# Performance work log

Hardware: AMD Instinct MI355X
Metric: run time of the kernel (lower is better)

The kernel has to match this reference:

```python
import jax, jax.numpy as jnp
import numpy as np

N_NODES = 50000
N_EDGES = 600000
VOCAB = 50000
D_IN = 256   # embed.output_size
D = 128      # size


def gcn_conv(x, w, b, src, dst, num_nodes):
    # PyG GCNConv: x' = D^{-1/2} (A + I) D^{-1/2} (x @ W^T) + b
    loop = jnp.arange(num_nodes)
    s = jnp.concatenate([src, loop])
    d = jnp.concatenate([dst, loop])
    x = x @ w.T                                           # [N, D]
    deg = jax.ops.segment_sum(jnp.ones_like(s, x.dtype), d, num_segments=num_nodes)
    dinv = jnp.where(deg > 0, jax.lax.rsqrt(deg), 0.0)
    norm = dinv[s] * dinv[d]                              # [E+N]
    msgs = x[s] * norm[:, None]                           # gather + scale
    out = jax.ops.segment_sum(msgs, d, num_segments=num_nodes)  # scatter-add
    return out + b


def setup_inputs() -> dict:
    key = jax.random.key(0)
    ks = jax.random.split(key, 7)
    node_tokens = jax.random.randint(ks[0], (N_NODES,), 0, VOCAB)
    edge_index = jax.random.randint(ks[1], (2, N_EDGES), 0, N_NODES)
    embed_table = jax.random.normal(ks[2], (VOCAB, D_IN), dtype=jnp.float32) * 0.02
    W_node_w = jax.random.normal(ks[3], (D, D_IN), dtype=jnp.float32) * 0.02
    W_node_b = jnp.zeros((D,), dtype=jnp.float32)
    w1 = jax.random.normal(ks[4], (D, D), dtype=jnp.float32) * 0.02
    b1 = jnp.zeros((D,), dtype=jnp.float32)
    w2 = jax.random.normal(ks[5], (D, D), dtype=jnp.float32) * 0.02
    b2 = jnp.zeros((D,), dtype=jnp.float32)
    return {"node_tokens": node_tokens, "edge_index": edge_index,
            "embed_table": embed_table, "W_node_w": W_node_w, "W_node_b": W_node_b,
            "w1": w1, "b1": b1, "w2": w2, "b2": b2}


def reference(node_tokens, edge_index, embed_table, W_node_w, W_node_b, w1, b1, w2, b2):
    src, dst = edge_index[0], edge_index[1]
    e = embed_table[node_tokens]                 # [N, D_IN] embedding lookup
    x = e @ W_node_w.T + W_node_b                # [N, D]
    x = gcn_conv(x, w1, b1, src, dst, N_NODES)
    x = jax.nn.relu(x)
    x = gcn_conv(x, w2, b2, src, dst, N_NODES)
    return x
```

## Files before the change

### kernel.cpp

```cpp
#include <hip/hip_runtime.h>
#include <hip/hip_bf16.h>

#define N_NODES 50000
#define N_EDGES 600000
#define D_IN 256
#define D 128

#define GEMM_BLOCKS ((N_NODES + 31) / 32)
#define EDGE_BLOCKS ((N_EDGES + 255) / 256)
#define OUT_CHUNKS (N_NODES / 16)
#define BCAP 32
#define OVF_CAP 2048

typedef unsigned short ushort_t;
typedef __attribute__((ext_vector_type(8))) short bf16x8;
typedef __attribute__((ext_vector_type(16))) float f32x16;

__device__ __forceinline__ float bf2f(ushort_t u) {
  union { unsigned int i; float f; } v;
  v.i = ((unsigned int)u) << 16;
  return v.f;
}
__device__ __forceinline__ ushort_t f2bf(float f) {
  union { float f; unsigned int i; } v;
  v.f = f;
  unsigned int x = v.i;
  unsigned int r = (x + 0x7FFFu + ((x >> 16) & 1u)) >> 16;
  return (ushort_t)r;
}
__device__ __forceinline__ float bflo(unsigned int u) {
  union { unsigned int i; float f; } v;
  v.i = u << 16;
  return v.f;
}
__device__ __forceinline__ float bfhi(unsigned int u) {
  union { unsigned int i; float f; } v;
  v.i = u & 0xFFFF0000u;
  return v.f;
}


__global__ __launch_bounds__(256) void k_prep_fill(
    const float* __restrict__ wn, const float* __restrict__ w1,
    const float* __restrict__ bn, const float* __restrict__ w2,
    const float* __restrict__ b1, const float* __restrict__ b2,
    const int* __restrict__ src, const int* __restrict__ dst,
    ushort_t* __restrict__ WcSw, ushort_t* __restrict__ W2Sw,
    float* __restrict__ bias_ws, int* __restrict__ deg,
    int* __restrict__ bucket, int* __restrict__ ovfc, int* __restrict__ ovf,
    ushort_t* __restrict__ T1z, ushort_t* __restrict__ T2z) {
  int bid = blockIdx.x;
  int tid = threadIdx.x;
  float* bcf = bias_ws;
  float* b1f = bias_ws + 128;
  float* b2f = bias_ws + 256;
  if (bid < 128) {
    int j = bid;
    int k = tid;
    float acc = 0.f;
#pragma unroll 8
    for (int m = 0; m < 128; m++)
      acc += w1[j * 128 + m] * wn[m * 256 + k];
    ushort_t h = f2bf(acc);
    ushort_t l = f2bf(acc - bf2f(h));
    int wv = j >> 5, fm = j & 31;
    int kh = k >> 7, t = (k >> 4) & 7, fq = (k >> 3) & 1, c = k & 7;
    int lane = fq * 32 + fm;
    int base = ((wv * 2 + kh) * 8 + t) * 2 * 512 + lane * 8 + c;
    WcSw[base] = h;
    WcSw[base + 512] = l;
    if (k == 0) {
      float s = 0.f;
      for (int m = 0; m < 128; m++) s += w1[j * 128 + m] * bn[m];
      bcf[j] = s;
    }
  } else if (bid < 193) {
    int i = (bid - 128) * 256 + tid;
    if (i < 16384) {
      float v = w2[i];
      ushort_t h = f2bf(v);
      ushort_t l = f2bf(v - bf2f(h));
      int j = i >> 7, k = i & 127;
      int wv = j >> 5, fm = j & 31;
      int t = (k >> 4) & 7, fq = (k >> 3) & 1, c = k & 7;
      int lane = fq * 32 + fm;
      int base = (wv * 8 + t) * 2 * 512 + lane * 8 + c;
      W2Sw[base] = h;
      W2Sw[base + 512] = l;
    } else if (i < 16512) {
      b1f[i - 16384] = b1[i - 16384];
    } else if (i < 16640) {
      b2f[i - 16512] = b2[i - 16512];
    }
  } else if (bid == 193) {
    unsigned int* z1 = (unsigned int*)&T1z[(size_t)N_NODES * D];
    unsigned int* z2 = (unsigned int*)&T2z[(size_t)N_NODES * D];
    if (tid < 64) z1[tid] = 0u;
    else if (tid < 128) z2[tid - 64] = 0u;
  } else {
    int e = (bid - 194) * 256 + tid;
    if (e < N_EDGES) {
      int d = dst[e];
      int s = src[e];
      int pos = atomicAdd(&deg[d], 1);
      if (pos < BCAP) {
        bucket[d * BCAP + pos] = s;
      } else {
        int oi = atomicAdd(ovfc, 1);
        if (oi < OVF_CAP) {
          ovf[2 * oi] = d;
          ovf[2 * oi + 1] = s;
        }
      }
    }
  }
}

__global__ __launch_bounds__(256) void k_gemm(
    const float* __restrict__ Xv, const int* __restrict__ tokens,
    const ushort_t* __restrict__ Wsw, const float* __restrict__ bias,
    const int* __restrict__ deg, ushort_t* __restrict__ OutT) {
  constexpr int XS = 136;
  __shared__ __align__(16) ushort_t xh_lds[32 * XS];
  __shared__ __align__(16) ushort_t xl_lds[32 * XS];

  int tid = threadIdx.x;
  int lane = tid & 63;
  int wv = tid >> 6;
  int node0 = blockIdx.x * 32;
  int fm = lane & 31;
  int fq = lane >> 5;
  int r8 = tid >> 5;
  int c32 = tid & 31;

  const char* xb = (const char*)Xv;
  float4 v0[4], v1[4];
  int rows[4];
#pragma unroll
  for (int i = 0; i < 4; i++) {
    rows[i] = r8 * 4 + i;
    int tk = tokens[min(node0 + rows[i], N_NODES - 1)];
    unsigned off = (unsigned)tk * (D_IN * 4) + (unsigned)c32 * 16;
    v0[i] = *(const float4*)(xb + off);
    v1[i] = *(const float4*)(xb + off + 512);
  }

  f32x16 acc;
#pragma unroll
  for (int r = 0; r < 16; r++) acc[r] = 0.f;

#pragma unroll
  for (int kh = 0; kh < 2; kh++) {
#pragma unroll
    for (int i = 0; i < 4; i++) {
      float4 v = (kh == 0) ? v0[i] : v1[i];
      ushort4 h, l;
      h.x = f2bf(v.x); l.x = f2bf(v.x - bf2f(h.x));
      h.y = f2bf(v.y); l.y = f2bf(v.y - bf2f(h.y));
      h.z = f2bf(v.z); l.z = f2bf(v.z - bf2f(h.z));
      h.w = f2bf(v.w); l.w = f2bf(v.w - bf2f(h.w));
      *(ushort4*)&xh_lds[rows[i] * XS + 4 * c32] = h;
      *(ushort4*)&xl_lds[rows[i] * XS + 4 * c32] = l;
    }
    __syncthreads();

    const ushort_t* wb = Wsw + ((size_t)(wv * 2 + kh) * 8) * 2 * 512 + lane * 8;
#pragma unroll
    for (int tc = 0; tc < 2; tc++) {
      bf16x8 wbh[4], wbl[4];
#pragma unroll
      for (int t4 = 0; t4 < 4; t4++) {
        wbh[t4] = *(const bf16x8*)(wb + (size_t)(tc * 4 + t4) * 1024);
        wbl[t4] = *(const bf16x8*)(wb + (size_t)(tc * 4 + t4) * 1024 + 512);
      }
#pragma unroll
      for (int t4 = 0; t4 < 4; t4++) {
        int ko = (tc * 4 + t4) * 16 + fq * 8;
        bf16x8 ah = *(const bf16x8*)&xh_lds[fm * XS + ko];
        bf16x8 al = *(const bf16x8*)&xl_lds[fm * XS + ko];
        acc = __builtin_amdgcn_mfma_f32_32x32x16_bf16(ah, wbh[t4], acc, 0, 0, 0);
        acc = __builtin_amdgcn_mfma_f32_32x32x16_bf16(ah, wbl[t4], acc, 0, 0, 0);
        acc = __builtin_amdgcn_mfma_f32_32x32x16_bf16(al, wbh[t4], acc, 0, 0, 0);
      }
    }
    if (kh == 0) __syncthreads();
  }

  int j = wv * 32 + fm;
  float bv = bias[j];
#pragma unroll
  for (int r = 0; r < 16; r++) {
    int row = (r & 3) + 8 * (r >> 2) + 4 * fq;
    int node = node0 + row;
    if (node < N_NODES) {
      float di = rsqrtf((float)(deg[node] + 1));
      OutT[(size_t)node * D + j] = f2bf((acc[r] + bv) * di);
    }
  }
}

__device__ __forceinline__ void addu4(float acc[8], uint4 u) {
  acc[0] += bflo(u.x);
  acc[1] += bfhi(u.x);
  acc[2] += bflo(u.y);
  acc[3] += bfhi(u.y);
  acc[4] += bflo(u.z);
  acc[5] += bfhi(u.z);
  acc[6] += bflo(u.w);
  acc[7] += bfhi(u.w);
}

__device__ __forceinline__ uint4 ldrow(const char* tbase, int s, int h) {
  return *(const uint4*)(tbase + (((unsigned)s << 8) + ((unsigned)h << 4)));
}

__device__ __forceinline__ void burst8(const char* tbase, int sidx,
                                       int gbase, int qoff, int h, float acc[8]) {
  uint4 u[8];
#pragma unroll
  for (int q = 0; q < 8; q++) {
    int s = __shfl(sidx, gbase + qoff + q);
    u[q] = ldrow(tbase, s, h);
  }
#pragma unroll
  for (int q = 0; q < 8; q++) addu4(acc, u[q]);
}

__device__ __forceinline__ void gather_node(
    const char* tbase, const int* __restrict__ bucket,
    const int* __restrict__ ovf, int novf,
    int node, int degv, bool valid, int gbase, int h, float acc[8]) {
  int cnt = valid ? min(degv, BCAP) : 0;
  addu4(acc, ldrow(tbase, valid ? node : N_NODES, h));
  int sidx = (h < cnt) ? bucket[node * BCAP + h] : N_NODES;
  burst8(tbase, sidx, gbase, 0, h, acc);
  burst8(tbase, sidx, gbase, 8, h, acc);
  for (int b2 = 16; b2 < cnt; b2 += 16) {
    int sx = (b2 + h < cnt) ? bucket[node * BCAP + b2 + h] : N_NODES;
    burst8(tbase, sx, gbase, 0, h, acc);
    burst8(tbase, sx, gbase, 8, h, acc);
  }
  if (valid && degv > BCAP) {
    for (int i = 0; i < novf; i++) {
      if (ovf[2 * i] == node) addu4(acc, ldrow(tbase, ovf[2 * i + 1], h));
    }
  }
}

__global__ __launch_bounds__(256) void k_agg_gemm(
    const ushort_t* __restrict__ t1, const int* __restrict__ deg,
    const int* __restrict__ bucket, const int* __restrict__ ovfc,
    const int* __restrict__ ovf, const float* __restrict__ b1f,
    const ushort_t* __restrict__ Wsw, ushort_t* __restrict__ OutT2) {
  constexpr int XS = 136;
  __shared__ __align__(16) ushort_t xh_lds[32 * XS];
  __shared__ __align__(16) ushort_t xl_lds[32 * XS];

  int tid = threadIdx.x;
  int lane = tid & 63;
  int wv = tid >> 6;
  int node0 = blockIdx.x * 32;
  int fm = lane & 31;
  int fq = lane >> 5;
  int g = lane >> 4;
  int h = lane & 15;
  int gbase = lane & 48;

  const char* tb = (const char*)t1;
  float4 bA = *(const float4*)&b1f[h * 8];
  float4 bB = *(const float4*)&b1f[h * 8 + 4];
  int novf = *ovfc;

  int node0w = node0 + wv * 8;
  int dgl = deg[min(node0w + min(lane, 7), N_NODES - 1)];

  int nodeA = node0w + g;
  int nodeB = node0w + 4 + g;
  int degA = __shfl(dgl, g);
  int degB = __shfl(dgl, 4 + g);
  bool vA = nodeA < N_NODES, vB = nodeB < N_NODES;
  float diA = rsqrtf((float)(degA + 1));
  float diB = rsqrtf((float)(degB + 1));

  float accA[8];
#pragma unroll
  for (int q = 0; q < 8; q++) accA[q] = 0.f;
  gather_node(tb, bucket, ovf, novf, nodeA, degA, vA, gbase, h, accA);

  float accB[8];
#pragma unroll
  for (int q = 0; q < 8; q++) accB[q] = 0.f;
  gather_node(tb, bucket, ovf, novf, nodeB, degB, vB, gbase, h, accB);

#pragma unroll
  for (int p = 0; p < 2; p++) {
    float* acc = p ? accB : accA;
    bool vv = p ? vB : vA;
    float di = p ? diB : diA;
    int row = wv * 8 + p * 4 + g;
    bf16x8 ph, pl;
    if (vv) {
      float val[8];
      val[0] = fmaxf(di * acc[0] + bA.x, 0.f);
      val[1] = fmaxf(di * acc[1] + bA.y, 0.f);
      val[2] = fmaxf(di * acc[2] + bA.z, 0.f);
      val[3] = fmaxf(di * acc[3] + bA.w, 0.f);
      val[4] = fmaxf(di * acc[4] + bB.x, 0.f);
      val[5] = fmaxf(di * acc[5] + bB.y, 0.f);
      val[6] = fmaxf(di * acc[6] + bB.z, 0.f);
      val[7] = fmaxf(di * acc[7] + bB.w, 0.f);
#pragma unroll
      for (int q = 0; q < 8; q++) {
        ushort_t hq = f2bf(val[q]);
        ph[q] = (short)hq;
        pl[q] = (short)f2bf(val[q] - bf2f(hq));
      }
    } else {
#pragma unroll
      for (int q = 0; q < 8; q++) { ph[q] = 0; pl[q] = 0; }
    }
    *(bf16x8*)&xh_lds[row * XS + h * 8] = ph;
    *(bf16x8*)&xl_lds[row * XS + h * 8] = pl;
  }
  __syncthreads();

  f32x16 acc;
#pragma unroll
  for (int r = 0; r < 16; r++) acc[r] = 0.f;
  {
    const ushort_t* wb = Wsw + ((size_t)wv * 8) * 2 * 512 + lane * 8;
#pragma unroll
    for (int tc = 0; tc < 2; tc++) {
      bf16x8 wbh[4], wbl[4];
#pragma unroll
      for (int t4 = 0; t4 < 4; t4++) {
        wbh[t4] = *(const bf16x8*)(wb + (size_t)(tc * 4 + t4) * 1024);
        wbl[t4] = *(const bf16x8*)(wb + (size_t)(tc * 4 + t4) * 1024 + 512);
      }
#pragma unroll
      for (int t4 = 0; t4 < 4; t4++) {
        int ko = (tc * 4 + t4) * 16 + fq * 8;
        bf16x8 ah = *(const bf16x8*)&xh_lds[fm * XS + ko];
        bf16x8 al = *(const bf16x8*)&xl_lds[fm * XS + ko];
        acc = __builtin_amdgcn_mfma_f32_32x32x16_bf16(ah, wbh[t4], acc, 0, 0, 0);
        acc = __builtin_amdgcn_mfma_f32_32x32x16_bf16(ah, wbl[t4], acc, 0, 0, 0);
        acc = __builtin_amdgcn_mfma_f32_32x32x16_bf16(al, wbh[t4], acc, 0, 0, 0);
      }
    }
  }
  int j = wv * 32 + fm;
#pragma unroll
  for (int r = 0; r < 16; r++) {
    int row = (r & 3) + 8 * (r >> 2) + 4 * fq;
    int node = node0 + row;
    if (node < N_NODES) {
      float di = rsqrtf((float)(deg[node] + 1));
      OutT2[(size_t)node * D + j] = f2bf(acc[r] * di);
    }
  }
}

__global__ __launch_bounds__(256) void k_agg_out(
    const ushort_t* __restrict__ t, const int* __restrict__ deg,
    const int* __restrict__ bucket, const int* __restrict__ ovfc,
    const int* __restrict__ ovf, const float* __restrict__ bias,
    float* __restrict__ out_f) {
  int wv = threadIdx.x >> 6;
  int lane = threadIdx.x & 63;
  int g = lane >> 4;
  int h = lane & 15;
  int gbase = lane & 48;
  int nodew = blockIdx.x * 16 + wv * 4;
  int dgl = deg[min(nodew + min(lane, 3), N_NODES - 1)];
  int node = nodew + g;
  int degn = __shfl(dgl, g);
  bool vn = node < N_NODES;
  float di = rsqrtf((float)(degn + 1));
  int novf = *ovfc;

  const char* tb = (const char*)t;
  float acc[8];
#pragma unroll
  for (int q = 0; q < 8; q++) acc[q] = 0.f;
  gather_node(tb, bucket, ovf, novf, node, degn, vn, gbase, h, acc);

  if (!vn) return;
  float4 bA = *(const float4*)&bias[h * 8];
  float4 bB = *(const float4*)&bias[h * 8 + 4];
  float4 o0, o1;
  o0.x = di * acc[0] + bA.x;
  o0.y = di * acc[1] + bA.y;
  o0.z = di * acc[2] + bA.z;
  o0.w = di * acc[3] + bA.w;
  o1.x = di * acc[4] + bB.x;
  o1.y = di * acc[5] + bB.y;
  o1.z = di * acc[6] + bB.z;
  o1.w = di * acc[7] + bB.w;
  *(float4*)&out_f[(size_t)node * D + h * 8] = o0;
  *(float4*)&out_f[(size_t)node * D + h * 8 + 4] = o1;
}

extern "C" void kernel_launch(void* const* d_in, const int* in_sizes, int n_in,
                              void* d_out, int out_size, void* d_ws, size_t ws_size,
                              hipStream_t stream) {
  const int* tokens = (const int*)d_in[0];
  const int* edge = (const int*)d_in[1];
  const float* embed = (const float*)d_in[2];
  const float* Wn = (const float*)d_in[3];
  const float* bn = (const float*)d_in[4];
  const float* w1 = (const float*)d_in[5];
  const float* b1 = (const float*)d_in[6];
  const float* w2 = (const float*)d_in[7];
  const float* b2 = (const float*)d_in[8];
  float* out = (float*)d_out;

  const int* src = edge;
  const int* dst = edge + N_EDGES;

  char* ws = (char*)d_ws;
  ushort_t* T1 = (ushort_t*)ws;
  ushort_t* T2 = (ushort_t*)(ws + 12800256);
  int* bucket = (int*)(ws + 25600512);
  int* deg = (int*)(ws + 32000512);
  int* ovfc = (int*)(ws + 32200512);
  int* ovf = (int*)(ws + 32200640);
  ushort_t* WcSw = (ushort_t*)(ws + 32217088);
  ushort_t* W2Sw = (ushort_t*)(ws + 32348160);
  float* bias_ws = (float*)(ws + 32413696);
  float* bcf = bias_ws;
  float* b1f = bias_ws + 128;
  float* b2f = bias_ws + 256;

  hipMemsetAsync(deg, 0, 200128, stream);

  k_prep_fill<<<194 + EDGE_BLOCKS, 256, 0, stream>>>(
      Wn, w1, bn, w2, b1, b2, src, dst, WcSw, W2Sw, bias_ws, deg,
      bucket, ovfc, ovf, T1, T2);

  k_gemm<<<GEMM_BLOCKS, 256, 0, stream>>>(
      embed, tokens, WcSw, bcf, deg, T1);

  k_agg_gemm<<<GEMM_BLOCKS, 256, 0, stream>>>(
      T1, deg, bucket, ovfc, ovf, b1f, W2Sw, T2);

  k_agg_out<<<OUT_CHUNKS, 256, 0, stream>>>(
      T2, deg, bucket, ovfc, ovf, b2f, out);
}
```

Baseline: 227.9 us.

## Fuse bucket fill into first GEMM and move degree scaling to gather

The edge-bucketing pass is merged into the embedding GEMM kernel using interleaved block roles, so the atomic scatter runs concurrently with the MFMA work instead of as a separate serial stage. Because the GEMM no longer has degree counts available, the source-side rsqrt(deg) normalization moves into the gather as a per-neighbor FMA scale. Bucket entries are stored as 16-bit indices to halve index traffic. This adds per-edge deg lookups and shuffles in the aggregation, and the 16-bit indices rely on node ids fitting in 16 bits. Since 50000 is below 65536 that holds, though the code does not check it.

```diff
diff --git a/kernel.cpp b/kernel.cpp
--- a/kernel.cpp
+++ b/kernel.cpp
@@ -8,6 +8,7 @@
 
 #define GEMM_BLOCKS ((N_NODES + 31) / 32)
 #define EDGE_BLOCKS ((N_EDGES + 255) / 256)
+#define MIX_BLOCKS 3910
 #define OUT_CHUNKS (N_NODES / 16)
 #define BCAP 32
 #define OVF_CAP 2048
@@ -40,14 +41,12 @@
 }
 
 
-__global__ __launch_bounds__(256) void k_prep_fill(
+__global__ __launch_bounds__(256) void k_wprep(
     const float* __restrict__ wn, const float* __restrict__ w1,
     const float* __restrict__ bn, const float* __restrict__ w2,
     const float* __restrict__ b1, const float* __restrict__ b2,
-    const int* __restrict__ src, const int* __restrict__ dst,
     ushort_t* __restrict__ WcSw, ushort_t* __restrict__ W2Sw,
-    float* __restrict__ bias_ws, int* __restrict__ deg,
-    int* __restrict__ bucket, int* __restrict__ ovfc, int* __restrict__ ovf,
+    float* __restrict__ bias_ws,
     ushort_t* __restrict__ T1z, ushort_t* __restrict__ T2z) {
   int bid = blockIdx.x;
   int tid = threadIdx.x;
@@ -92,19 +91,38 @@
     } else if (i < 16640) {
       b2f[i - 16512] = b2[i - 16512];
     }
-  } else if (bid == 193) {
+  } else {
     unsigned int* z1 = (unsigned int*)&T1z[(size_t)N_NODES * D];
     unsigned int* z2 = (unsigned int*)&T2z[(size_t)N_NODES * D];
     if (tid < 64) z1[tid] = 0u;
     else if (tid < 128) z2[tid - 64] = 0u;
-  } else {
-    int e = (bid - 194) * 256 + tid;
+  }
+}
+
+__global__ __launch_bounds__(256) void k_gemm_fill(
+    const float* __restrict__ Xv, const int* __restrict__ tokens,
+    const ushort_t* __restrict__ Wsw, const float* __restrict__ bias,
+    ushort_t* __restrict__ OutT,
+    const int* __restrict__ src, const int* __restrict__ dst,
+    int* __restrict__ deg, ushort_t* __restrict__ bucket,
+    int* __restrict__ ovfc, int* __restrict__ ovf) {
+  constexpr int XS = 136;
+  __shared__ __align__(16) ushort_t xh_lds[32 * XS];
+  __shared__ __align__(16) ushort_t xl_lds[32 * XS];
+
+  int bid = blockIdx.x;
+  int tid = threadIdx.x;
+  int grp = bid / 5, r = bid % 5;
+  if (r >= 2) {
+    int c = grp * 3 + (r - 2);
+    if (c >= EDGE_BLOCKS) return;
+    int e = c * 256 + tid;
     if (e < N_EDGES) {
       int d = dst[e];
       int s = src[e];
       int pos = atomicAdd(&deg[d], 1);
       if (pos < BCAP) {
-        bucket[d * BCAP + pos] = s;
+        bucket[d * BCAP + pos] = (ushort_t)s;
       } else {
         int oi = atomicAdd(ovfc, 1);
         if (oi < OVF_CAP) {
@@ -113,21 +131,14 @@
         }
       }
     }
-  }
-}
-
-__global__ __launch_bounds__(256) void k_gemm(
-    const float* __restrict__ Xv, const int* __restrict__ tokens,
-    const ushort_t* __restrict__ Wsw, const float* __restrict__ bias,
-    const int* __restrict__ deg, ushort_t* __restrict__ OutT) {
-  constexpr int XS = 136;
-  __shared__ __align__(16) ushort_t xh_lds[32 * XS];
-  __shared__ __align__(16) ushort_t xl_lds[32 * XS];
-
-  int tid = threadIdx.x;
+    return;
+  }
+
+  int t = grp * 2 + r;
+  if (t >= GEMM_BLOCKS) return;
   int lane = tid & 63;
   int wv = tid >> 6;
-  int node0 = blockIdx.x * 32;
+  int node0 = t * 32;
   int fm = lane & 31;
   int fq = lane >> 5;
   int r8 = tid >> 5;
@@ -147,7 +158,7 @@
 
   f32x16 acc;
 #pragma unroll
-  for (int r = 0; r < 16; r++) acc[r] = 0.f;
+  for (int q = 0; q < 16; q++) acc[q] = 0.f;
 
 #pragma unroll
   for (int kh = 0; kh < 2; kh++) {
@@ -189,67 +200,71 @@
   int j = wv * 32 + fm;
   float bv = bias[j];
 #pragma unroll
-  for (int r = 0; r < 16; r++) {
-    int row = (r & 3) + 8 * (r >> 2) + 4 * fq;
+  for (int q = 0; q < 16; q++) {
+    int row = (q & 3) + 8 * (q >> 2) + 4 * fq;
     int node = node0 + row;
-    if (node < N_NODES) {
-      float di = rsqrtf((float)(deg[node] + 1));
-      OutT[(size_t)node * D + j] = f2bf((acc[r] + bv) * di);
-    }
-  }
-}
-
-__device__ __forceinline__ void addu4(float acc[8], uint4 u) {
-  acc[0] += bflo(u.x);
-  acc[1] += bfhi(u.x);
-  acc[2] += bflo(u.y);
-  acc[3] += bfhi(u.y);
-  acc[4] += bflo(u.z);
-  acc[5] += bfhi(u.z);
-  acc[6] += bflo(u.w);
-  acc[7] += bfhi(u.w);
+    if (node < N_NODES)
+      OutT[(size_t)node * D + j] = f2bf(acc[q] + bv);
+  }
+}
+
+__device__ __forceinline__ void fma8(float acc[8], uint4 u, float f) {
+  acc[0] = fmaf(bflo(u.x), f, acc[0]);
+  acc[1] = fmaf(bfhi(u.x), f, acc[1]);
+  acc[2] = fmaf(bflo(u.y), f, acc[2]);
+  acc[3] = fmaf(bfhi(u.y), f, acc[3]);
+  acc[4] = fmaf(bflo(u.z), f, acc[4]);
+  acc[5] = fmaf(bfhi(u.z), f, acc[5]);
+  acc[6] = fmaf(bflo(u.w), f, acc[6]);
+  acc[7] = fmaf(bfhi(u.w), f, acc[7]);
 }
 
 __device__ __forceinline__ uint4 ldrow(const char* tbase, int s, int h) {
   return *(const uint4*)(tbase + (((unsigned)s << 8) + ((unsigned)h << 4)));
 }
 
-__device__ __forceinline__ void burst8(const char* tbase, int sidx,
-                                       int gbase, int qoff, int h, float acc[8]) {
+__device__ __forceinline__ void burst8s(const char* tbase, int sidx, float scl,
+                                        int gbase, int qoff, int h, float acc[8]) {
   uint4 u[8];
+  float f[8];
 #pragma unroll
   for (int q = 0; q < 8; q++) {
     int s = __shfl(sidx, gbase + qoff + q);
+    f[q] = __shfl(scl, gbase + qoff + q);
     u[q] = ldrow(tbase, s, h);
   }
 #pragma unroll
-  for (int q = 0; q < 8; q++) addu4(acc, u[q]);
+  for (int q = 0; q < 8; q++) fma8(acc, u[q], f[q]);
 }
 
 __device__ __forceinline__ void gather_node(
-    const char* tbase, const int* __restrict__ bucket,
-    const int* __restrict__ ovf, int novf,
+    const char* tbase, const ushort_t* __restrict__ bucket,
+    const int* __restrict__ deg, const int* __restrict__ ovf, int novf,
     int node, int degv, bool valid, int gbase, int h, float acc[8]) {
   int cnt = valid ? min(degv, BCAP) : 0;
-  addu4(acc, ldrow(tbase, valid ? node : N_NODES, h));
-  int sidx = (h < cnt) ? bucket[node * BCAP + h] : N_NODES;
-  burst8(tbase, sidx, gbase, 0, h, acc);
-  burst8(tbase, sidx, gbase, 8, h, acc);
+  int sidx = (h < cnt) ? (int)bucket[node * BCAP + h] : N_NODES;
+  float scl = rsqrtf((float)(deg[sidx] + 1));
+  burst8s(tbase, sidx, scl, gbase, 0, h, acc);
+  burst8s(tbase, sidx, scl, gbase, 8, h, acc);
   for (int b2 = 16; b2 < cnt; b2 += 16) {
-    int sx = (b2 + h < cnt) ? bucket[node * BCAP + b2 + h] : N_NODES;
-    burst8(tbase, sx, gbase, 0, h, acc);
-    burst8(tbase, sx, gbase, 8, h, acc);
+    int sx = (b2 + h < cnt) ? (int)bucket[node * BCAP + b2 + h] : N_NODES;
+    float sc = rsqrtf((float)(deg[sx] + 1));
+    burst8s(tbase, sx, sc, gbase, 0, h, acc);
+    burst8s(tbase, sx, sc, gbase, 8, h, acc);
   }
   if (valid && degv > BCAP) {
     for (int i = 0; i < novf; i++) {
-      if (ovf[2 * i] == node) addu4(acc, ldrow(tbase, ovf[2 * i + 1], h));
+      if (ovf[2 * i] == node) {
+        int s = ovf[2 * i + 1];
+        fma8(acc, ldrow(tbase, s, h), rsqrtf((float)(deg[s] + 1)));
+      }
     }
   }
 }
 
 __global__ __launch_bounds__(256) void k_agg_gemm(
     const ushort_t* __restrict__ t1, const int* __restrict__ deg,
-    const int* __restrict__ bucket, const int* __restrict__ ovfc,
+    const ushort_t* __restrict__ bucket, const int* __restrict__ ovfc,
     const int* __restrict__ ovf, const float* __restrict__ b1f,
     const ushort_t* __restrict__ Wsw, ushort_t* __restrict__ OutT2) {
   constexpr int XS = 136;
@@ -285,12 +300,14 @@
   float accA[8];
 #pragma unroll
   for (int q = 0; q < 8; q++) accA[q] = 0.f;
-  gather_node(tb, bucket, ovf, novf, nodeA, degA, vA, gbase, h, accA);
+  fma8(accA, ldrow(tb, vA ? nodeA : N_NODES, h), diA);
+  gather_node(tb, bucket, deg, ovf, novf, nodeA, degA, vA, gbase, h, accA);
 
   float accB[8];
 #pragma unroll
   for (int q = 0; q < 8; q++) accB[q] = 0.f;
-  gather_node(tb, bucket, ovf, novf, nodeB, degB, vB, gbase, h, accB);
+  fma8(accB, ldrow(tb, vB ? nodeB : N_NODES, h), diB);
+  gather_node(tb, bucket, deg, ovf, novf, nodeB, degB, vB, gbase, h, accB);
 
 #pragma unroll
   for (int p = 0; p < 2; p++) {
@@ -326,7 +343,7 @@
 
   f32x16 acc;
 #pragma unroll
-  for (int r = 0; r < 16; r++) acc[r] = 0.f;
+  for (int q = 0; q < 16; q++) acc[q] = 0.f;
   {
     const ushort_t* wb = Wsw + ((size_t)wv * 8) * 2 * 512 + lane * 8;
 #pragma unroll
@@ -350,19 +367,17 @@
   }
   int j = wv * 32 + fm;
 #pragma unroll
-  for (int r = 0; r < 16; r++) {
-    int row = (r & 3) + 8 * (r >> 2) + 4 * fq;
+  for (int q = 0; q < 16; q++) {
+    int row = (q & 3) + 8 * (q >> 2) + 4 * fq;
     int node = node0 + row;
-    if (node < N_NODES) {
-      float di = rsqrtf((float)(deg[node] + 1));
-      OutT2[(size_t)node * D + j] = f2bf(acc[r] * di);
-    }
+    if (node < N_NODES)
+      OutT2[(size_t)node * D + j] = f2bf(acc[q]);
   }
 }
 
 __global__ __launch_bounds__(256) void k_agg_out(
     const ushort_t* __restrict__ t, const int* __restrict__ deg,
-    const int* __restrict__ bucket, const int* __restrict__ ovfc,
+    const ushort_t* __restrict__ bucket, const int* __restrict__ ovfc,
     const int* __restrict__ ovf, const float* __restrict__ bias,
     float* __restrict__ out_f) {
   int wv = threadIdx.x >> 6;
@@ -382,7 +397,8 @@
   float acc[8];
 #pragma unroll
   for (int q = 0; q < 8; q++) acc[q] = 0.f;
-  gather_node(tb, bucket, ovf, novf, node, degn, vn, gbase, h, acc);
+  fma8(acc, ldrow(tb, vn ? node : N_NODES, h), di);
+  gather_node(tb, bucket, deg, ovf, novf, node, degn, vn, gbase, h, acc);
 
   if (!vn) return;
   float4 bA = *(const float4*)&bias[h * 8];
@@ -420,25 +436,24 @@
   char* ws = (char*)d_ws;
   ushort_t* T1 = (ushort_t*)ws;
   ushort_t* T2 = (ushort_t*)(ws + 12800256);
-  int* bucket = (int*)(ws + 25600512);
-  int* deg = (int*)(ws + 32000512);
-  int* ovfc = (int*)(ws + 32200512);
-  int* ovf = (int*)(ws + 32200640);
-  ushort_t* WcSw = (ushort_t*)(ws + 32217088);
-  ushort_t* W2Sw = (ushort_t*)(ws + 32348160);
-  float* bias_ws = (float*)(ws + 32413696);
+  ushort_t* bucket = (ushort_t*)(ws + 25600512);
+  int* deg = (int*)(ws + 28800512);
+  int* ovfc = (int*)(ws + 29000576);
+  int* ovf = (int*)(ws + 29000704);
+  ushort_t* WcSw = (ushort_t*)(ws + 29017088);
+  ushort_t* W2Sw = (ushort_t*)(ws + 29148160);
+  float* bias_ws = (float*)(ws + 29213696);
   float* bcf = bias_ws;
   float* b1f = bias_ws + 128;
   float* b2f = bias_ws + 256;
 
-  hipMemsetAsync(deg, 0, 200128, stream);
-
-  k_prep_fill<<<194 + EDGE_BLOCKS, 256, 0, stream>>>(
-      Wn, w1, bn, w2, b1, b2, src, dst, WcSw, W2Sw, bias_ws, deg,
-      bucket, ovfc, ovf, T1, T2);
-
-  k_gemm<<<GEMM_BLOCKS, 256, 0, stream>>>(
-      embed, tokens, WcSw, bcf, deg, T1);
+  hipMemsetAsync(deg, 0, 200192, stream);
+
+  k_wprep<<<194, 256, 0, stream>>>(
+      Wn, w1, bn, w2, b1, b2, WcSw, W2Sw, bias_ws, T1, T2);
+
+  k_gemm_fill<<<MIX_BLOCKS, 256, 0, stream>>>(
+      embed, tokens, WcSw, bcf, T1, src, dst, deg, bucket, ovfc, ovf);
 
   k_agg_gemm<<<GEMM_BLOCKS, 256, 0, stream>>>(
       T1, deg, bucket, ovfc, ovf, b1f, W2Sw, T2);
```

Measured after the change: 214.6 us. 5.9% less time.
